# Optimization experiments

Hardware: AMD Instinct MI355X
Metric: run time of the kernel (lower is better)

The kernel has to match this reference:

```python
import jax, jax.numpy as jnp
import numpy as np

OBS_DIM, ACT_DIM, HID_DIM, FEAT = 256, 32, 1024, 512
T_STEPS, BATCH = 64, 512
LOG2PI = float(np.log(2.0 * np.pi))


def _mlp(h, w0, b0, w1, b1, w2, b2):
    # 2 hidden elu layers + linear head (MLPDecoder mean; fix_std Normal, std=1)
    x = jax.nn.elu(h @ w0.T + b0)
    x = jax.nn.elu(x @ w1.T + b1)
    return x @ w2.T + b2


def _gru(x, h, w_ih, w_hh, b_ih, b_hh):
    # torch.nn.GRUCell semantics
    gi = x @ w_ih.T + b_ih
    gh = h @ w_hh.T + b_hh
    i_r, i_z, i_n = jnp.split(gi, 3, axis=-1)
    h_r, h_z, h_n = jnp.split(gh, 3, axis=-1)
    r = jax.nn.sigmoid(i_r + h_r)
    z = jax.nn.sigmoid(i_z + h_z)
    n = jnp.tanh(i_n + r * h_n)
    return (1.0 - z) * n + z * h


def setup_inputs() -> dict:
    key = jax.random.key(0)
    ks = jax.random.split(key, 20)
    d = {}
    d['obs'] = jax.random.normal(ks[0], (T_STEPS, BATCH, OBS_DIM), jnp.float32)
    d['action'] = jax.random.normal(ks[1], (T_STEPS, BATCH, ACT_DIM), jnp.float32)
    d['reward'] = jax.random.normal(ks[2], (T_STEPS, BATCH, 1), jnp.float32)
    in_dim = OBS_DIM + ACT_DIM
    s = lambda fan_in: 1.0 / np.sqrt(fan_in)
    d['gru_w_ih'] = jax.random.normal(ks[3], (3 * HID_DIM, in_dim), jnp.float32) * s(in_dim)
    d['gru_w_hh'] = jax.random.normal(ks[4], (3 * HID_DIM, HID_DIM), jnp.float32) * s(HID_DIM)
    d['gru_b_ih'] = jnp.zeros((3 * HID_DIM,), jnp.float32)
    d['gru_b_hh'] = jnp.zeros((3 * HID_DIM,), jnp.float32)
    for name, out_dim, base in (('obs', OBS_DIM, 5), ('rew', 1, 11)):
        d[f'{name}_w0'] = jax.random.normal(ks[base], (FEAT, HID_DIM), jnp.float32) * s(HID_DIM)
        d[f'{name}_b0'] = jnp.zeros((FEAT,), jnp.float32)
        d[f'{name}_w1'] = jax.random.normal(ks[base + 1], (FEAT, FEAT), jnp.float32) * s(FEAT)
        d[f'{name}_b1'] = jnp.zeros((FEAT,), jnp.float32)
        d[f'{name}_w2'] = jax.random.normal(ks[base + 2], (out_dim, FEAT), jnp.float32) * s(FEAT)
        d[f'{name}_b2'] = jnp.zeros((out_dim,), jnp.float32)
    return d


def reference(obs, action, reward,
              gru_w_ih, gru_w_hh, gru_b_ih, gru_b_hh,
              obs_w0, obs_b0, obs_w1, obs_b1, obs_w2, obs_b2,
              rew_w0, rew_b0, rew_w1, rew_b1, rew_w2, rew_b2):
    T, B = obs.shape[0], obs.shape[1]

    def normal_logprob_sum(x, mean):
        # Normal(mean, std=1): -0.5*(x-mean)^2 - 0.5*log(2*pi), summed
        return -0.5 * jnp.sum((x - mean) ** 2 + LOG2PI)

    h0 = _gru(jnp.concatenate([obs[0], jnp.zeros_like(action[0])], axis=1),
              jnp.zeros((B, HID_DIM), obs.dtype),
              gru_w_ih, gru_w_hh, gru_b_ih, gru_b_hh)

    def step(h, xs):
        obs_t, act_t, rew_t = xs
        obs_mean = _mlp(h, obs_w0, obs_b0, obs_w1, obs_b1, obs_w2, obs_b2)
        lp_obs = normal_logprob_sum(obs_t, obs_mean)
        rew_mean = _mlp(h, rew_w0, rew_b0, rew_w1, rew_b1, rew_w2, rew_b2)
        lp_rew = normal_logprob_sum(rew_t, rew_mean)
        # feed predicted obs (mode) + ground-truth action back into the GRU
        x = jnp.concatenate([obs_mean, act_t], axis=1)
        h_next = _gru(x, h, gru_w_ih, gru_w_hh, gru_b_ih, gru_b_hh)
        return h_next, (obs_mean, rew_mean, lp_obs, lp_rew)

    _, (pre_obs, pre_reward, lp_obs, lp_rew) = jax.lax.scan(
        step, h0, (obs, action, reward))

    denom = jnp.asarray(T * B, obs.dtype)
    pre_obs_loss = -jnp.sum(lp_obs) / denom
    pre_reward_loss = -jnp.sum(lp_rew) / denom
    loss = pre_obs_loss + pre_reward_loss  # action_mimic=False -> action loss is 0
    return loss, pre_obs, pre_reward
```

## Files before the change

### kernel.cpp

```cpp
#include <hip/hip_runtime.h>
#include <stdint.h>

#define T_STEPS 64
#define BATCH   512
#define OBS_DIM 256
#define ACT_DIM 32
#define HID     1024
#define FEAT    512
#define GDIM    3072
#define KIH     288
#define NBLK    256
#define GMEMB   32
#define LOG2PI  1.8378770664093453f
#define HWREG_XCC_ID 14356

typedef __attribute__((ext_vector_type(8))) short  short8;
typedef __attribute__((ext_vector_type(4))) float  floatx4;
typedef __attribute__((ext_vector_type(4))) unsigned int uintx4;
typedef unsigned long long ull;

__device__ __forceinline__ float bf2f(unsigned int u) {
    return __uint_as_float(u << 16);
}
__device__ __forceinline__ unsigned int f2bf(float f) {
    unsigned int u = __float_as_uint(f);
    return (u + 0x7FFFu + ((u >> 16) & 1u)) >> 16;
}
__device__ __forceinline__ float elu1(float x)  { return x > 0.f ? x : expm1f(x); }
__device__ __forceinline__ float sigm(float x)  { return 1.f / (1.f + expf(-x)); }

__device__ __forceinline__ unsigned int dev_ld(const unsigned int* p) {
    return __hip_atomic_load(p, __ATOMIC_RELAXED, __HIP_MEMORY_SCOPE_AGENT);
}
__device__ __forceinline__ ull dev_ld64(const ull* p) {
    return __hip_atomic_load(p, __ATOMIC_RELAXED, __HIP_MEMORY_SCOPE_AGENT);
}
__device__ __forceinline__ void dev_st(unsigned int* p, unsigned int v) {
    __hip_atomic_store(p, v, __ATOMIC_RELAXED, __HIP_MEMORY_SCOPE_AGENT);
}
__device__ __forceinline__ float dev_ldf(const float* p) {
    return __uint_as_float(dev_ld((const unsigned int*)p));
}

template<bool COH>
__device__ __forceinline__ unsigned int a_ld(const unsigned int* p) {
    return COH ? dev_ld(p) : *p;
}
template<bool COH>
__device__ __forceinline__ ull a_ld64(const ull* p) {
    return COH ? dev_ld64(p) : *p;
}
template<bool COH>
__device__ __forceinline__ void a_st(unsigned int* p, unsigned int v) {
    if (COH) dev_st(p, v); else *p = v;
}

struct ParamsReal {
    const float* obs; const float* action; const float* reward;
    const float* b_ih; const float* b_hh;
    const float* b1o; const float* b1r; const float* b2o; const float* b2r;
    const unsigned short* Ws1; const unsigned short* Wih;
    const unsigned short* W1o; const unsigned short* W1r;
    const unsigned short* W2o; const unsigned short* w2r;
    const float* bias_s1;
    unsigned short* Z1[2]; unsigned short* Z2[2]; unsigned short* Xbuf[2];
    unsigned short* hbf[2]; unsigned short* GHb[2]; float* h[2];
    float* accum; float* out;
    int* bar;
};
#define P ParamsReal

__device__ __forceinline__ void bar_fast() {
    asm volatile("" ::: "memory");
    __builtin_amdgcn_s_barrier();
    asm volatile("" ::: "memory");
}
__device__ __forceinline__ void bar_lds() {
    asm volatile("s_waitcnt lgkmcnt(0)" ::: "memory");
    __builtin_amdgcn_s_barrier();
    asm volatile("" ::: "memory");
}

__device__ __forceinline__ void gbar(int* cnt, int* gen, int& epoch, int members) {
    __syncthreads();
    if (threadIdx.x == 0) {
        __builtin_amdgcn_fence(__ATOMIC_RELEASE, "workgroup");
        epoch++;
        int prev = __hip_atomic_fetch_add(cnt, 1, __ATOMIC_RELAXED,
                                          __HIP_MEMORY_SCOPE_AGENT);
        if (prev == members * epoch - 1) {
            __hip_atomic_store(gen, epoch, __ATOMIC_RELAXED,
                               __HIP_MEMORY_SCOPE_AGENT);
        } else {
            while (__hip_atomic_load(gen, __ATOMIC_RELAXED,
                                     __HIP_MEMORY_SCOPE_AGENT) < epoch)
                __builtin_amdgcn_s_sleep(2);
        }
        __builtin_amdgcn_fence(__ATOMIC_ACQUIRE, "workgroup");
    }
    __syncthreads();
}

template<bool COH>
__device__ __forceinline__ void s1_stage(const P& p, unsigned short* lds,
                                         int g, int m,
                                         const unsigned short* hbf_r,
                                         unsigned short* Z1_w,
                                         unsigned short* GHb_w) {
    const int tid = threadIdx.x, lane = tid & 63, wv = tid >> 6;
    const int wr = wv & 1, wc = wv >> 1, fr = lane & 15, fq = lane >> 4;
    const int rowg = g * 64, col0 = m * 128;
    unsigned short* ldsA = lds;
    unsigned short* ldsB = lds + 64 * 136;

    floatx4 acc[2][4];
    floatx4 z4 = {0.f, 0.f, 0.f, 0.f};
#pragma unroll
    for (int mi = 0; mi < 2; ++mi)
#pragma unroll
        for (int n = 0; n < 4; ++n) acc[mi][n] = z4;

    const ull* Aq = (const ull*)(hbf_r + (size_t)rowg * HID);
    const unsigned short* Bg = p.Ws1 + (size_t)col0 * HID;

    ull apf[8];
#pragma unroll
    for (int j = 0; j < 8; ++j) { int f = tid + 256 * j;
        apf[j] = a_ld64<COH>(Aq + (size_t)(f >> 5) * 256 + (f & 31)); }
    uintx4 rb0[4], rb1[4];
#pragma unroll
    for (int i = 0; i < 4; ++i) { int c = tid + 256 * i;
        const unsigned short* bp = Bg + (size_t)(c >> 3) * HID + ((c & 7) << 3);
        rb0[i] = __builtin_nontemporal_load((const uintx4*)bp);
        rb1[i] = __builtin_nontemporal_load((const uintx4*)(bp + 64)); }

#define S1_MFMA(ASUB)                                                          \
    {                                                                          \
        _Pragma("unroll")                                                      \
        for (int ks = 0; ks < 2; ++ks) {                                       \
            short8 af[2], bf8[4];                                              \
            _Pragma("unroll")                                                  \
            for (int mi = 0; mi < 2; ++mi)                                     \
                af[mi] = *(const short8*)(ldsA + (wr * 32 + mi * 16 + fr) * 136 + (ASUB) + ks * 32 + fq * 8); \
            _Pragma("unroll")                                                  \
            for (int n = 0; n < 4; ++n)                                        \
                bf8[n] = *(const short8*)(ldsB + (wc * 64 + n * 16 + fr) * 72 + ks * 32 + fq * 8); \
            _Pragma("unroll")                                                  \
            for (int mi = 0; mi < 2; ++mi)                                     \
                _Pragma("unroll")                                              \
                for (int n = 0; n < 4; ++n)                                    \
                    acc[mi][n] = __builtin_amdgcn_mfma_f32_16x16x32_bf16(      \
                        af[mi], bf8[n], acc[mi][n], 0, 0, 0);                  \
        }                                                                      \
// ... 36 lines not shown
    }
#undef S1_MFMA

    const bool isZ1 = (col0 < 1024);
#pragma unroll
    for (int mi = 0; mi < 2; ++mi)
#pragma unroll
        for (int n = 0; n < 4; ++n)
#pragma unroll
            for (int j = 0; j < 4; ++j) {
                int row = rowg + wr * 32 + mi * 16 + fq * 4 + j;
                int col = col0 + wc * 64 + n * 16 + fr;
                float v = acc[mi][n][j] + p.bias_s1[col];
                unsigned int ow = f2bf(isZ1 ? elu1(v) : v);
                unsigned int pr = __shfl_xor(ow, 1, 64);
                if (!(fr & 1)) {
                    unsigned int pk = ow | (pr << 16);
                    if (isZ1)
                        a_st<COH>((unsigned int*)(Z1_w + row * HID + col), pk);
                    else
                        a_st<COH>((unsigned int*)GHb_w + (size_t)row * 1536 + ((col - 1024) >> 1), pk);
                }
            }
}

template<bool COH>
__device__ __forceinline__ void s2_stage(const P& p, unsigned short* lds,
                                         int g, int m,
                                         const unsigned short* Z1_r,
                                         unsigned short* Z2_w) {
    const int tid = threadIdx.x, lane = tid & 63, wv = tid >> 6;
    const int wr = wv & 1, wc = wv >> 1, fr = lane & 15, fq = lane >> 4;
    const int rowg = g * 64;
    const int z = m >> 4, col0 = (m & 15) * 32;
    unsigned short* ldsA = lds;
    unsigned short* ldsB = lds + 64 * 136;

    floatx4 acc[2];
    floatx4 z4 = {0.f, 0.f, 0.f, 0.f};
    acc[0] = z4; acc[1] = z4;

    const ull* Aq = (const ull*)(Z1_r + (size_t)rowg * HID + z * FEAT);
    const unsigned short* Bg = (z ? p.W1r : p.W1o) + (size_t)col0 * FEAT;
    const float* bias = z ? p.b1r : p.b1o;

    ull apf[8];
#pragma unroll
    for (int j = 0; j < 8; ++j) { int f = tid + 256 * j;
        apf[j] = a_ld64<COH>(Aq + (size_t)(f >> 5) * 256 + (f & 31)); }
    const unsigned short* bp0 = Bg + (size_t)(tid >> 3) * FEAT + ((tid & 7) << 3);
    uintx4 rb0 = *(const uintx4*)(bp0);
    uintx4 rb1 = *(const uintx4*)(bp0 + 64);

#define S2_MFMA(ASUB)                                                          \
    {                                                                          \
        _Pragma("unroll")                                                      \
        for (int ks = 0; ks < 2; ++ks) {                                       \
            short8 bf8 = *(const short8*)(ldsB + (wc * 16 + fr) * 72 + ks * 32 + fq * 8); \
            _Pragma("unroll")                                                  \
            for (int mi = 0; mi < 2; ++mi) {                                   \
                short8 af = *(const short8*)(ldsA + (wr * 32 + mi * 16 + fr) * 136 + (ASUB) + ks * 32 + fq * 8); \
                acc[mi] = __builtin_amdgcn_mfma_f32_16x16x32_bf16(af, bf8, acc[mi], 0, 0, 0); \
            }                                                                  \
        }                                                                      \
    }

    for (int it2 = 0; it2 < 4; ++it2) {
        bar_fast();
#pragma unroll
        for (int j = 0; j < 8; ++j) { int f = tid + 256 * j;
            *(ull*)(ldsA + (size_t)(f >> 5) * 136 + ((f & 31) << 2)) = apf[j]; }
        *(uintx4*)(ldsB + (tid >> 3) * 72 + ((tid & 7) << 3)) = rb0;
        bar_lds();
        if (it2 < 3) {
            int c2 = it2 + 1;
#pragma unroll
            for (int j = 0; j < 8; ++j) { int f = tid + 256 * j;
                apf[j] = a_ld64<COH>(Aq + (size_t)(f >> 5) * 256 + c2 * 32 + (f & 31)); }
            rb0 = *(const uintx4*)(bp0 + (2 * it2 + 2) * 64);
        }
        S2_MFMA(0);
        bar_fast();
        *(uintx4*)(ldsB + (tid >> 3) * 72 + ((tid & 7) << 3)) = rb1;
        bar_lds();
        if (it2 < 3) rb1 = *(const uintx4*)(bp0 + (2 * it2 + 3) * 64);
        S2_MFMA(64);
    }
#undef S2_MFMA

#pragma unroll
    for (int mi = 0; mi < 2; ++mi)
#pragma unroll
        for (int j = 0; j < 4; ++j) {
            int row = rowg + wr * 32 + mi * 16 + fq * 4 + j;
            int col = col0 + wc * 16 + fr;
            float v = acc[mi][j] + bias[col];
            unsigned int ow = f2bf(elu1(v));
            unsigned int pr = __shfl_xor(ow, 1, 64);
            if (!(fr & 1))
                a_st<COH>((unsigned int*)(Z2_w + row * HID + z * FEAT + col), ow | (pr << 16));
        }
}

template<bool COH>
__device__ __forceinline__ void s3_stage(const P& p, unsigned short* lds,
                                         int g, int m, int t,
                                         const unsigned short* Z2_r,
                                         unsigned short* Xbuf_w) {
    const int tid = threadIdx.x, lane = tid & 63, wv = tid >> 6;
    const int wr = wv & 1, wc = wv >> 1, fr = lane & 15, fq = lane >> 4;
    const int rowg = g * 64;

    if (m < 8) {
        const int col0 = m * 32;
        unsigned short* ldsA = lds;
        unsigned short* ldsB = lds + 64 * 136;
        floatx4 acc[2];
        floatx4 z4 = {0.f, 0.f, 0.f, 0.f};
        acc[0] = z4; acc[1] = z4;

        const ull* Aq = (const ull*)(Z2_r + (size_t)rowg * HID);
        const unsigned short* Bg = p.W2o + (size_t)col0 * FEAT;

        ull apf[8];
#pragma unroll
        for (int j = 0; j < 8; ++j) { int f = tid + 256 * j;
            apf[j] = a_ld64<COH>(Aq + (size_t)(f >> 5) * 256 + (f & 31)); }
        const unsigned short* bp0 = Bg + (size_t)(tid >> 3) * FEAT + ((tid & 7) << 3);
        uintx4 rb0 = *(const uintx4*)(bp0);
        uintx4 rb1 = *(const uintx4*)(bp0 + 64);

#define S3_MFMA(ASUB)                                                          \
        {                                                                      \
            _Pragma("unroll")                                                  \
            for (int ks = 0; ks < 2; ++ks) {                                   \
                short8 bf8 = *(const short8*)(ldsB + (wc * 16 + fr) * 72 + ks * 32 + fq * 8); \
                _Pragma("unroll")                                              \
                for (int mi = 0; mi < 2; ++mi) {                               \
                    short8 af = *(const short8*)(ldsA + (wr * 32 + mi * 16 + fr) * 136 + (ASUB) + ks * 32 + fq * 8); \
                    acc[mi] = __builtin_amdgcn_mfma_f32_16x16x32_bf16(af, bf8, acc[mi], 0, 0, 0); \
                }                                                              \
            }                                                                  \
        }

        for (int it2 = 0; it2 < 4; ++it2) {
            bar_fast();
#pragma unroll
            for (int j = 0; j < 8; ++j) { int f = tid + 256 * j;
                *(ull*)(ldsA + (size_t)(f >> 5) * 136 + ((f & 31) << 2)) = apf[j]; }
            *(uintx4*)(ldsB + (tid >> 3) * 72 + ((tid & 7) << 3)) = rb0;
            bar_lds();
            if (it2 < 3) {
                int c2 = it2 + 1;
#pragma unroll
                for (int j = 0; j < 8; ++j) { int f = tid + 256 * j;
                    apf[j] = a_ld64<COH>(Aq + (size_t)(f >> 5) * 256 + c2 * 32 + (f & 31)); }
                rb0 = *(const uintx4*)(bp0 + (2 * it2 + 2) * 64);
            }
            S3_MFMA(0);
            bar_fast();
            *(uintx4*)(ldsB + (tid >> 3) * 72 + ((tid & 7) << 3)) = rb1;
            bar_lds();
            if (it2 < 3) rb1 = *(const uintx4*)(bp0 + (2 * it2 + 3) * 64);
            S3_MFMA(64);
        }
#undef S3_MFMA

        const int col = col0 + wc * 16 + fr;
        const float b2oc = p.b2o[col];
        float lsum = 0.f;
#pragma unroll
        for (int mi = 0; mi < 2; ++mi)
#pragma unroll
            for (int j = 0; j < 4; ++j) {
                int row = rowg + wr * 32 + mi * 16 + fq * 4 + j;
                float mval = acc[mi][j] + b2oc;
                size_t oidx = (size_t)t * BATCH * OBS_DIM + (size_t)row * OBS_DIM + col;
                __builtin_nontemporal_store(mval, p.out + 1 + oidx);
                unsigned int ow = f2bf(mval);
                unsigned int pr = __shfl_xor(ow, 1, 64);
                if (!(fr & 1))
                    a_st<COH>((unsigned int*)(Xbuf_w + row * KIH + col), ow | (pr << 16));
                float d = __builtin_nontemporal_load(p.obs + oidx) - mval;
                lsum += d * d;
            }
#pragma unroll
        for (int off = 32; off > 0; off >>= 1) lsum += __shfl_down(lsum, off, 64);
        if (lane == 0) atomicAdd(p.accum + 0, lsum);
    } else if (m == 8) {
        for (int e = tid; e < 64 * 16; e += 256) {
            int row = rowg + (e >> 4), cp = (e & 15) * 2;
            const float* ap = p.action + ((size_t)t * BATCH + row) * ACT_DIM + cp;
            unsigned int lo = f2bf(__builtin_nontemporal_load(ap));
            unsigned int hi = f2bf(__builtin_nontemporal_load(ap + 1));
            a_st<COH>((unsigned int*)(Xbuf_w + row * KIH + OBS_DIM + cp), lo | (hi << 16));
        }
    } else if (m >= 16) {
        const int row = rowg + (m - 16) * 4 + wv;
        const ull* zq = (const ull*)(Z2_r + (size_t)row * HID + FEAT) + lane * 2;
        ull z0 = a_ld64<COH>(zq);
        ull z1 = a_ld64<COH>(zq + 1);
        short8 w8 = *(const short8*)(p.w2r + lane * 8);
        float s = 0.f;
#pragma unroll
        for (int k = 0; k < 4; ++k) {
            unsigned int u = (unsigned int)(z0 >> (16 * k)) & 0xFFFFu;
            s += bf2f(u) * bf2f((unsigned int)(unsigned short)w8[k]);
        }
#pragma unroll
        for (int k = 0; k < 4; ++k) {
            unsigned int u = (unsigned int)(z1 >> (16 * k)) & 0xFFFFu;
            s += bf2f(u) * bf2f((unsigned int)(unsigned short)w8[4 + k]);
        }
#pragma unroll
        for (int off = 32; off > 0; off >>= 1) s += __shfl_down(s, off, 64);
        if (lane == 0) {
            float mm = s + p.b2r[0];
            __builtin_nontemporal_store(
                mm, p.out + 1 + (size_t)T_STEPS * BATCH * OBS_DIM + (size_t)t * BATCH + row);
            float d = __builtin_nontemporal_load(p.reward + (size_t)t * BATCH + row) - mm;
            atomicAdd(p.accum + 1, d * d);
        }
    }
}

template<bool COH>
__device__ __forceinline__ void s4_stage(const P& p, unsigned short* lds,
                                         int g, int m, int use_gh,
                                         const unsigned short* Xbuf_r,
                                         const unsigned short* GHb_r,
                                         const float* h_r,
                                         float* h_w, unsigned short* hbf_w) {
    const int tid = threadIdx.x, lane = tid & 63, wv = tid >> 6;
    const int wr = wv & 1, wc = wv >> 1, fr = lane & 15, fq = lane >> 4;
    const int rowg = g * 64;
    const int col0 = m * 32;
    unsigned short* ldsA = lds;
    unsigned short* ldsB = lds + 64 * 104;

    floatx4 acc[3][2];
    floatx4 z4 = {0.f, 0.f, 0.f, 0.f};
#pragma unroll
    for (int g3 = 0; g3 < 3; ++g3) { acc[g3][0] = z4; acc[g3][1] = z4; }

    const ull* Xq = (const ull*)(Xbuf_r + (size_t)rowg * KIH);
    ull apf[6];
#pragma unroll
    for (int j = 0; j < 6; ++j) { int f = tid + 256 * j;
        apf[j] = a_ld64<COH>(Xq + (size_t)(f / 24) * 72 + (f % 24)); }

    uintx4 wpfA[5], wpfB[5];
#pragma unroll
    for (int j = 0; j < 5; ++j) { int f = tid + 256 * j;
        if (f < 1152) { int r = f / 12, ko = (f - r * 12) * 8;
            const unsigned short* wp =
                p.Wih + (size_t)((r >> 5) * HID + col0 + (r & 31)) * KIH + ko;
            wpfA[j] = __builtin_nontemporal_load((const uintx4*)wp);
            wpfB[j] = __builtin_nontemporal_load((const uintx4*)(wp + 96)); } }

#pragma unroll
    for (int c = 0; c < 3; ++c) {
        bar_fast();
#pragma unroll
        for (int j = 0; j < 6; ++j) { int f = tid + 256 * j;
            *(ull*)(ldsA + (size_t)(f / 24) * 104 + ((f % 24) << 2)) = apf[j]; }
#pragma unroll
        for (int j = 0; j < 5; ++j) { int f = tid + 256 * j;
            if (f < 1152) { int r = f / 12, ko = (f - r * 12) * 8;
                *(uintx4*)(ldsB + r * 104 + ko) = (c & 1) ? wpfB[j] : wpfA[j]; } }
        bar_lds();
        if (c < 2) {
#pragma unroll
            for (int j = 0; j < 6; ++j) { int f = tid + 256 * j;
                apf[j] = a_ld64<COH>(Xq + (size_t)(f / 24) * 72 + (c + 1) * 24 + (f % 24)); }
        }
        if (c == 0) {
#pragma unroll
            for (int j = 0; j < 5; ++j) { int f = tid + 256 * j;
                if (f < 1152) { int r = f / 12, ko = (f - r * 12) * 8;
                    wpfA[j] = __builtin_nontemporal_load((const uintx4*)
                        (p.Wih + (size_t)((r >> 5) * HID + col0 + (r & 31)) * KIH + 192 + ko)); } }
        }
#pragma unroll
        for (int ks = 0; ks < 3; ++ks) {
            short8 af[2];
#pragma unroll
            for (int mi = 0; mi < 2; ++mi)
                af[mi] = *(const short8*)(ldsA + (wr * 32 + mi * 16 + fr) * 104 + ks * 32 + fq * 8);
#pragma unroll
            for (int g3 = 0; g3 < 3; ++g3) {
                short8 bf8 = *(const short8*)(ldsB + (g3 * 32 + wc * 16 + fr) * 104 + ks * 32 + fq * 8);
#pragma unroll
                for (int mi = 0; mi < 2; ++mi)
                    acc[g3][mi] = __builtin_amdgcn_mfma_f32_16x16x32_bf16(
                        af[mi], bf8, acc[g3][mi], 0, 0, 0);
            }
        }
    }

    const int col = col0 + wc * 16 + fr;
    const float bir = p.b_ih[col];
    const float biz = p.b_ih[HID + col];
    const float bin = p.b_ih[2 * HID + col];
    float hrv[2][4], hzv[2][4], hnv[2][4], hpv[2][4];
    if (use_gh) {
        const unsigned int* GW = (const unsigned int*)GHb_r;
        const int cw = col >> 1, hi = col & 1;
#pragma unroll
        for (int mi = 0; mi < 2; ++mi)
#pragma unroll
            for (int j = 0; j < 4; ++j) {
                int row = rowg + wr * 32 + mi * 16 + fq * 4 + j;
                unsigned int ur = a_ld<COH>(GW + (size_t)row * 1536 + cw);
                unsigned int uz = a_ld<COH>(GW + (size_t)row * 1536 + 512 + cw);
                unsigned int un = a_ld<COH>(GW + (size_t)row * 1536 + 1024 + cw);
                hrv[mi][j] = bf2f(hi ? (ur >> 16) : (ur & 0xFFFFu));
                hzv[mi][j] = bf2f(hi ? (uz >> 16) : (uz & 0xFFFFu));
                hnv[mi][j] = bf2f(hi ? (un >> 16) : (un & 0xFFFFu));
                hpv[mi][j] = __uint_as_float(a_ld<COH>((const unsigned int*)(h_r + (size_t)row * HID + col)));
            }
    } else {
        float br = p.b_hh[col], bz = p.b_hh[HID + col], bn = p.b_hh[2 * HID + col];
#pragma unroll
        for (int mi = 0; mi < 2; ++mi)
#pragma unroll
            for (int j = 0; j < 4; ++j) {
                hrv[mi][j] = br; hzv[mi][j] = bz; hnv[mi][j] = bn; hpv[mi][j] = 0.f;
            }
    }
#pragma unroll
    for (int mi = 0; mi < 2; ++mi)
#pragma unroll
        for (int j = 0; j < 4; ++j) {
            int row = rowg + wr * 32 + mi * 16 + fq * 4 + j;
            float r  = sigm(acc[0][mi][j] + bir + hrv[mi][j]);
            float z  = sigm(acc[1][mi][j] + biz + hzv[mi][j]);
            float nn = tanhf(acc[2][mi][j] + bin + r * hnv[mi][j]);
            float hv = (1.f - z) * nn + z * hpv[mi][j];
            a_st<COH>((unsigned int*)(h_w + (size_t)row * HID + col), __float_as_uint(hv));
            unsigned int ow = f2bf(hv);
            unsigned int pr = __shfl_xor(ow, 1, 64);
            if (!(fr & 1))
                a_st<COH>((unsigned int*)(hbf_w + row * HID + col), ow | (pr << 16));
        }
}

template<bool COH>
__device__ void rollout(const P& p, unsigned short* lds, int g, int m) {
    int* gcnt = p.bar + g * 128;
    int* ggen = p.bar + g * 128 + 64;
    int epoch = 0;

    s4_stage<COH>(p, lds, g, m, 0, p.Xbuf[1], p.GHb[0], p.h[0], p.h[0], p.hbf[0]);
    gbar(gcnt, ggen, epoch, GMEMB);

    for (int t = 0; t < T_STEPS; ++t) {
        const int pr = t & 1, nx = (t + 1) & 1;
        s1_stage<COH>(p, lds, g, m, p.hbf[pr], p.Z1[pr], p.GHb[pr]);
        gbar(gcnt, ggen, epoch, GMEMB);
        s2_stage<COH>(p, lds, g, m, p.Z1[pr], p.Z2[pr]);
        gbar(gcnt, ggen, epoch, GMEMB);
        s3_stage<COH>(p, lds, g, m, t, p.Z2[pr], p.Xbuf[pr]);
        gbar(gcnt, ggen, epoch, GMEMB);
        if (t < T_STEPS - 1) {
            s4_stage<COH>(p, lds, g, m, 1, p.Xbuf[pr], p.GHb[pr], p.h[pr],
                          p.h[nx], p.hbf[nx]);
            gbar(gcnt, ggen, epoch, GMEMB);
        }
    }
}

__global__ __launch_bounds__(256, 1) void k_persist(P p) {
    __shared__ unsigned short lds[17920];
    __shared__ int sh[3];

    const int bid = blockIdx.x;
    if (threadIdx.x == 0) {
        unsigned int xcd = __builtin_amdgcn_s_getreg(HWREG_XCC_ID) & 7u;
        int r = __hip_atomic_fetch_add(p.bar + 1024 + xcd, 1,
                                       __ATOMIC_RELAXED, __HIP_MEMORY_SCOPE_AGENT);
        sh[0] = (int)xcd; sh[1] = r;
    }
    int repoch = 0;
    gbar(p.bar + 1200, p.bar + 1264, repoch, NBLK);
    if (threadIdx.x == 0) {
        int ok = (sh[1] < 32);
        for (int i = 0; i < 8; ++i)
            ok &= (dev_ld((const unsigned int*)(p.bar + 1024 + i)) == 32u);
        sh[2] = ok;
    }
    __syncthreads();

    if (sh[2]) rollout<false>(p, lds, sh[0], sh[1]);
    else       rollout<true >(p, lds, bid & 7, bid >> 3);

    gbar(p.bar + 1200, p.bar + 1264, repoch, NBLK);
    if (bid == 0 && threadIdx.x == 0) {
        const float inv = 1.f / (float)(T_STEPS * BATCH);
        float a0 = dev_ldf(p.accum + 0);
        float a1 = dev_ldf(p.accum + 1);
        p.out[0] = 0.5f * a0 * inv + 128.f * LOG2PI
                 + 0.5f * a1 * inv + 0.5f * LOG2PI;
    }
}

__global__ void k_convert(
    const float* __restrict__ ow0, const float* __restrict__ rw0,
    const float* __restrict__ whh, const float* __restrict__ wih,
    const float* __restrict__ ow1, const float* __restrict__ rw1,
    const float* __restrict__ ow2, const float* __restrict__ rw2,
    const float* __restrict__ ob0, const float* __restrict__ rb0,
    const float* __restrict__ bhh,
    unsigned short* __restrict__ Ws1, unsigned short* __restrict__ Wih,
    unsigned short* __restrict__ W1o, unsigned short* __restrict__ W1r,
    unsigned short* __restrict__ W2o, unsigned short* __restrict__ w2r,
    float* __restrict__ bias_s1)
{
    const int i0 = blockIdx.x * 256 + threadIdx.x;
    const int stride = gridDim.x * 256;
    for (int i = i0; i < 4096 * 1024; i += stride) {
        int row = i >> 10;
        float v = (row < 512) ? ow0[i]
                : (row < 1024) ? rw0[i - 512 * 1024]
                               : whh[i - 1024 * 1024];
        Ws1[i] = (unsigned short)f2bf(v);
    }
    for (int i = i0; i < GDIM * KIH; i += stride) Wih[i] = (unsigned short)f2bf(wih[i]);
    for (int i = i0; i < FEAT * FEAT; i += stride) {
        W1o[i] = (unsigned short)f2bf(ow1[i]);
        W1r[i] = (unsigned short)f2bf(rw1[i]);
    }
    for (int i = i0; i < OBS_DIM * FEAT; i += stride) W2o[i] = (unsigned short)f2bf(ow2[i]);
    for (int i = i0; i < FEAT; i += stride) w2r[i] = (unsigned short)f2bf(rw2[i]);
    for (int i = i0; i < 4096; i += stride)
        bias_s1[i] = (i < 512) ? ob0[i] : (i < 1024) ? rb0[i - 512] : bhh[i - 1024];
}

__global__ void k_init(const float* __restrict__ obs,
                       unsigned short* __restrict__ Xbuf1,
                       float* __restrict__ accum,
                       int* __restrict__ bar)
{
    int i = blockIdx.x * 256 + threadIdx.x;
    if (i < BATCH * KIH) {
        int row = i / KIH, col = i - row * KIH;
        Xbuf1[i] = (col < OBS_DIM) ? (unsigned short)f2bf(obs[row * OBS_DIM + col])
                                   : (unsigned short)0;
    }
    if (i < 2)    accum[i] = 0.f;
    if (i < 1536) bar[i] = 0;
}

extern "C" void kernel_launch(void* const* d_in, const int* in_sizes, int n_in,
                              void* d_out, int out_size, void* d_ws, size_t ws_size,
                              hipStream_t stream)
{
    const float* obs      = (const float*)d_in[0];
    const float* action   = (const float*)d_in[1];
    const float* reward   = (const float*)d_in[2];
    const float* gru_w_ih = (const float*)d_in[3];
    const float* gru_w_hh = (const float*)d_in[4];
    const float* gru_b_ih = (const float*)d_in[5];
    const float* gru_b_hh = (const float*)d_in[6];
    const float* obs_w0   = (const float*)d_in[7];
    const float* obs_b0   = (const float*)d_in[8];
    const float* obs_w1   = (const float*)d_in[9];
    const float* obs_b1   = (const float*)d_in[10];
    const float* obs_w2   = (const float*)d_in[11];
    const float* obs_b2   = (const float*)d_in[12];
    const float* rew_w0   = (const float*)d_in[13];
    const float* rew_b0   = (const float*)d_in[14];
    const float* rew_w1   = (const float*)d_in[15];
    const float* rew_b1   = (const float*)d_in[16];
    const float* rew_w2   = (const float*)d_in[17];
    const float* rew_b2   = (const float*)d_in[18];

    char* ws = (char*)d_ws;
    auto alloc = [&](size_t bytes) -> char* {
        char* pr = ws;
        ws += (bytes + 255) & ~(size_t)255;
        return pr;
    };
    unsigned short* Ws1  = (unsigned short*)alloc((size_t)4096 * 1024 * 2);
    unsigned short* Wih  = (unsigned short*)alloc((size_t)GDIM * KIH * 2);
    unsigned short* W1o  = (unsigned short*)alloc((size_t)FEAT * FEAT * 2);
    unsigned short* W1r  = (unsigned short*)alloc((size_t)FEAT * FEAT * 2);
    unsigned short* W2o  = (unsigned short*)alloc((size_t)OBS_DIM * FEAT * 2);
    unsigned short* w2r  = (unsigned short*)alloc((size_t)FEAT * 2);
    float* bias_s1       = (float*)alloc((size_t)4096 * 4);
    unsigned short* Z1a  = (unsigned short*)alloc((size_t)BATCH * HID * 2);
    unsigned short* Z1b  = (unsigned short*)alloc((size_t)BATCH * HID * 2);
    unsigned short* Z2a  = (unsigned short*)alloc((size_t)BATCH * HID * 2);
    unsigned short* Z2b  = (unsigned short*)alloc((size_t)BATCH * HID * 2);
    unsigned short* GHa  = (unsigned short*)alloc((size_t)BATCH * GDIM * 2);
    unsigned short* GHbB = (unsigned short*)alloc((size_t)BATCH * GDIM * 2);
    unsigned short* Xba  = (unsigned short*)alloc((size_t)BATCH * KIH * 2);
    unsigned short* Xbb  = (unsigned short*)alloc((size_t)BATCH * KIH * 2);
    float* ha            = (float*)alloc((size_t)BATCH * HID * 4);
    float* hb            = (float*)alloc((size_t)BATCH * HID * 4);
    unsigned short* hfa  = (unsigned short*)alloc((size_t)BATCH * HID * 2);
    unsigned short* hfb  = (unsigned short*)alloc((size_t)BATCH * HID * 2);
    float* accum         = (float*)alloc(256);
    int*   bar           = (int*)alloc(8192);

    dim3 blk(256);

    k_convert<<<dim3(1024), blk, 0, stream>>>(
        obs_w0, rew_w0, gru_w_hh, gru_w_ih, obs_w1, rew_w1, obs_w2, rew_w2,
        obs_b0, rew_b0, gru_b_hh, Ws1, Wih, W1o, W1r, W2o, w2r, bias_s1);

    k_init<<<dim3((BATCH * KIH + 255) / 256), blk, 0, stream>>>(obs, Xbb, accum, bar);

    P hp;
    hp.obs = obs; hp.action = action; hp.reward = reward;
    hp.b_ih = gru_b_ih; hp.b_hh = gru_b_hh;
    hp.b1o = obs_b1; hp.b1r = rew_b1; hp.b2o = obs_b2; hp.b2r = rew_b2;
    hp.Ws1 = Ws1; hp.Wih = Wih; hp.W1o = W1o; hp.W1r = W1r;
    hp.W2o = W2o; hp.w2r = w2r; hp.bias_s1 = bias_s1;
    hp.Z1[0] = Z1a; hp.Z1[1] = Z1b;
    hp.Z2[0] = Z2a; hp.Z2[1] = Z2b;
    hp.Xbuf[0] = Xba; hp.Xbuf[1] = Xbb;
    hp.hbf[0] = hfa; hp.hbf[1] = hfb;
    hp.GHb[0] = GHa; hp.GHb[1] = GHbB;
    hp.h[0] = ha; hp.h[1] = hb;
    hp.accum = accum; hp.out = (float*)d_out;
    hp.bar = bar;

    k_persist<<<dim3(NBLK), blk, 0, stream>>>(hp);
}
```

Baseline: 2.542 ms.

## Fold obs head into GRU input weights and overlap head stage with GRU update

Precomputes a fused weight Wf = W_ih[:, :256]·W2o, plus a folded bias, in the convert kernel. The GRU input-gate GEMM can then read the second hidden layer Z2 directly instead of waiting for the obs-mean output stage. The s3 head/loss stage now runs between arrive and wait of a split flag barrier, so one full grid barrier per step leaves the critical path. The atomic counter barrier is replaced with per-block flag slots, and double buffers are collapsed to single buffers. In exchange the GRU input GEMM K grows from 288 to 544, setup runs a naive fp32 weight-product loop, and bf16 rounding of the folded weights changes numerics slightly.

```diff
diff --git a/kernel.cpp b/kernel.cpp
--- a/kernel.cpp
+++ b/kernel.cpp
@@ -9,6 +9,7 @@
 #define FEAT    512
 #define GDIM    3072
 #define KIH     288
+#define KF      544
 #define NBLK    256
 #define GMEMB   32
 #define LOG2PI  1.8378770664093453f
@@ -62,9 +63,10 @@
     const unsigned short* Ws1; const unsigned short* Wih;
     const unsigned short* W1o; const unsigned short* W1r;
     const unsigned short* W2o; const unsigned short* w2r;
+    const unsigned short* Wf;  const float* bf_fold;
     const float* bias_s1;
-    unsigned short* Z1[2]; unsigned short* Z2[2]; unsigned short* Xbuf[2];
-    unsigned short* hbf[2]; unsigned short* GHb[2]; float* h[2];
+    unsigned short* Z1; unsigned short* Z2; unsigned short* Xbuf1;
+    unsigned short* hbf; unsigned short* GHb; float* h[2];
     float* accum; float* out;
     int* bar;
 };
@@ -99,6 +101,28 @@
         __builtin_amdgcn_fence(__ATOMIC_ACQUIRE, "workgroup");
     }
     __syncthreads();
+}
+
+__device__ __forceinline__ void arrive_flags(int* fbase, int m, int epoch) {
+    __syncthreads();
+    if (threadIdx.x == 0) {
+        __builtin_amdgcn_fence(__ATOMIC_RELEASE, "workgroup");
+        dev_st((unsigned int*)(fbase + m * 16), (unsigned int)epoch);
+    }
+}
+__device__ __forceinline__ void wait_flags(int* fbase, int epoch) {
+    if (threadIdx.x < 64) {
+        const unsigned int* fp =
+            (const unsigned int*)(fbase + (threadIdx.x & 31) * 16);
+        while ((int)dev_ld(fp) < epoch) __builtin_amdgcn_s_sleep(4);
+        __builtin_amdgcn_fence(__ATOMIC_ACQUIRE, "workgroup");
+    }
+    __syncthreads();
+}
+__device__ __forceinline__ void gbar_flags(int* fbase, int m, int& epoch) {
+    epoch++;
+    arrive_flags(fbase, m, epoch);
+    wait_flags(fbase, epoch);
 }
 
 template<bool COH>
@@ -241,18 +265,16 @@
     uintx4 rb0 = *(const uintx4*)(bp0);
     uintx4 rb1 = *(const uintx4*)(bp0 + 64);
 
-#define S2_MFMA(ASUB)                                                          \
-    {                                                                          \
+#define S23_MFMA(ASUB)                                                         \
+    { _Pragma("unroll")                                                        \
+      for (int ks = 0; ks < 2; ++ks) {                                         \
+        short8 bf8 = *(const short8*)(ldsB + (wc * 16 + fr) * 72 + ks * 32 + fq * 8); \
         _Pragma("unroll")                                                      \
-        for (int ks = 0; ks < 2; ++ks) {                                       \
-            short8 bf8 = *(const short8*)(ldsB + (wc * 16 + fr) * 72 + ks * 32 + fq * 8); \
-            _Pragma("unroll")                                                  \
-            for (int mi = 0; mi < 2; ++mi) {                                   \
-                short8 af = *(const short8*)(ldsA + (wr * 32 + mi * 16 + fr) * 136 + (ASUB) + ks * 32 + fq * 8); \
-                acc[mi] = __builtin_amdgcn_mfma_f32_16x16x32_bf16(af, bf8, acc[mi], 0, 0, 0); \
-            }                                                                  \
+        for (int mi = 0; mi < 2; ++mi) {                                       \
+            short8 af = *(const short8*)(ldsA + (wr * 32 + mi * 16 + fr) * 136 + (ASUB) + ks * 32 + fq * 8); \
+            acc[mi] = __builtin_amdgcn_mfma_f32_16x16x32_bf16(af, bf8, acc[mi], 0, 0, 0); \
         }                                                                      \
-    }
+      } }
 
     for (int it2 = 0; it2 < 4; ++it2) {
         bar_fast();
@@ -268,14 +290,13 @@
                 apf[j] = a_ld64<COH>(Aq + (size_t)(f >> 5) * 256 + c2 * 32 + (f & 31)); }
             rb0 = *(const uintx4*)(bp0 + (2 * it2 + 2) * 64);
         }
-        S2_MFMA(0);
+        S23_MFMA(0);
         bar_fast();
         *(uintx4*)(ldsB + (tid >> 3) * 72 + ((tid & 7) << 3)) = rb1;
         bar_lds();
         if (it2 < 3) rb1 = *(const uintx4*)(bp0 + (2 * it2 + 3) * 64);
-        S2_MFMA(64);
-    }
-#undef S2_MFMA
+        S23_MFMA(64);
+    }
 
 #pragma unroll
     for (int mi = 0; mi < 2; ++mi)
@@ -294,10 +315,10 @@
 template<bool COH>
 __device__ __forceinline__ void s3_stage(const P& p, unsigned short* lds,
                                          int g, int m, int t,
-                                         const unsigned short* Z2_r,
-                                         unsigned short* Xbuf_w) {
+                                         const unsigned short* Z2_r) {
     const int tid = threadIdx.x, lane = tid & 63, wv = tid >> 6;
-    const int wr = wv & 1, wc = wv >> 1, fr = lane & 15, fq = lane >> 4;
+    const int wr = wv & 1, wc = wv >> 1;
+    const int fr = lane & 15, fq = lane >> 4;
     const int rowg = g * 64;
 
     if (m < 8) {
@@ -319,19 +340,6 @@
         uintx4 rb0 = *(const uintx4*)(bp0);
         uintx4 rb1 = *(const uintx4*)(bp0 + 64);
 
-#define S3_MFMA(ASUB)                                                          \
-        {                                                                      \
-            _Pragma("unroll")                                                  \
-            for (int ks = 0; ks < 2; ++ks) {                                   \
-                short8 bf8 = *(const short8*)(ldsB + (wc * 16 + fr) * 72 + ks * 32 + fq * 8); \
-                _Pragma("unroll")                                              \
-                for (int mi = 0; mi < 2; ++mi) {                               \
-                    short8 af = *(const short8*)(ldsA + (wr * 32 + mi * 16 + fr) * 136 + (ASUB) + ks * 32 + fq * 8); \
-                    acc[mi] = __builtin_amdgcn_mfma_f32_16x16x32_bf16(af, bf8, acc[mi], 0, 0, 0); \
-                }                                                              \
-            }                                                                  \
-        }
-
         for (int it2 = 0; it2 < 4; ++it2) {
             bar_fast();
 #pragma unroll
@@ -346,14 +354,13 @@
                     apf[j] = a_ld64<COH>(Aq + (size_t)(f >> 5) * 256 + c2 * 32 + (f & 31)); }
                 rb0 = *(const uintx4*)(bp0 + (2 * it2 + 2) * 64);
             }
-            S3_MFMA(0);
+            S23_MFMA(0);
             bar_fast();
             *(uintx4*)(ldsB + (tid >> 3) * 72 + ((tid & 7) << 3)) = rb1;
             bar_lds();
             if (it2 < 3) rb1 = *(const uintx4*)(bp0 + (2 * it2 + 3) * 64);
-            S3_MFMA(64);
-        }
-#undef S3_MFMA
+            S23_MFMA(64);
+        }
 
         const int col = col0 + wc * 16 + fr;
         const float b2oc = p.b2o[col];
@@ -366,24 +373,12 @@
                 float mval = acc[mi][j] + b2oc;
                 size_t oidx = (size_t)t * BATCH * OBS_DIM + (size_t)row * OBS_DIM + col;
                 __builtin_nontemporal_store(mval, p.out + 1 + oidx);
-                unsigned int ow = f2bf(mval);
-                unsigned int pr = __shfl_xor(ow, 1, 64);
-                if (!(fr & 1))
-                    a_st<COH>((unsigned int*)(Xbuf_w + row * KIH + col), ow | (pr << 16));
                 float d = __builtin_nontemporal_load(p.obs + oidx) - mval;
                 lsum += d * d;
             }
 #pragma unroll
         for (int off = 32; off > 0; off >>= 1) lsum += __shfl_down(lsum, off, 64);
         if (lane == 0) atomicAdd(p.accum + 0, lsum);
-    } else if (m == 8) {
-        for (int e = tid; e < 64 * 16; e += 256) {
-            int row = rowg + (e >> 4), cp = (e & 15) * 2;
-            const float* ap = p.action + ((size_t)t * BATCH + row) * ACT_DIM + cp;
-            unsigned int lo = f2bf(__builtin_nontemporal_load(ap));
-            unsigned int hi = f2bf(__builtin_nontemporal_load(ap + 1));
-            a_st<COH>((unsigned int*)(Xbuf_w + row * KIH + OBS_DIM + cp), lo | (hi << 16));
-        }
     } else if (m >= 16) {
         const int row = rowg + (m - 16) * 4 + wv;
         const ull* zq = (const ull*)(Z2_r + (size_t)row * HID + FEAT) + lane * 2;
@@ -414,85 +409,134 @@
 }
 
 template<bool COH>
-__device__ __forceinline__ void s4_stage(const P& p, unsigned short* lds,
-                                         int g, int m, int use_gh,
-                                         const unsigned short* Xbuf_r,
-                                         const unsigned short* GHb_r,
-                                         const float* h_r,
-                                         float* h_w, unsigned short* hbf_w) {
+__device__ __forceinline__ void s4f_stage(const P& p, unsigned short* lds,
+                                          int g, int m, int t,
+                                          const unsigned short* Z2_r,
+                                          const unsigned short* GHb_r,
+                                          const float* h_r,
+                                          float* h_w, unsigned short* hbf_w) {
     const int tid = threadIdx.x, lane = tid & 63, wv = tid >> 6;
-    const int wr = wv & 1, wc = wv >> 1, fr = lane & 15, fq = lane >> 4;
+    const int wr = wv & 1, wc = wv >> 1;
+    const int fr = lane & 15, fq = lane >> 4;
     const int rowg = g * 64;
     const int col0 = m * 32;
     unsigned short* ldsA = lds;
-    unsigned short* ldsB = lds + 64 * 104;
+    unsigned short* ldsB = lds + 64 * 136;
 
     floatx4 acc[3][2];
     floatx4 z4 = {0.f, 0.f, 0.f, 0.f};
 #pragma unroll
     for (int g3 = 0; g3 < 3; ++g3) { acc[g3][0] = z4; acc[g3][1] = z4; }
 
-    const ull* Xq = (const ull*)(Xbuf_r + (size_t)rowg * KIH);
-    ull apf[6];
-#pragma unroll
-    for (int j = 0; j < 6; ++j) { int f = tid + 256 * j;
-        apf[j] = a_ld64<COH>(Xq + (size_t)(f / 24) * 72 + (f % 24)); }
-
-    uintx4 wpfA[5], wpfB[5];
-#pragma unroll
-    for (int j = 0; j < 5; ++j) { int f = tid + 256 * j;
-        if (f < 1152) { int r = f / 12, ko = (f - r * 12) * 8;
-            const unsigned short* wp =
-                p.Wih + (size_t)((r >> 5) * HID + col0 + (r & 31)) * KIH + ko;
-            wpfA[j] = __builtin_nontemporal_load((const uintx4*)wp);
-            wpfB[j] = __builtin_nontemporal_load((const uintx4*)(wp + 96)); } }
-
-#pragma unroll
-    for (int c = 0; c < 3; ++c) {
+    const ull* Aq = (const ull*)(Z2_r + (size_t)rowg * HID);
+
+    ull apf[8];
+#pragma unroll
+    for (int j = 0; j < 8; ++j) { int f = tid + 256 * j;
+        apf[j] = a_ld64<COH>(Aq + (size_t)(f >> 5) * 256 + (f & 31)); }
+    uintx4 rb0[3], rb1[3];
+#pragma unroll
+    for (int i = 0; i < 3; ++i) { int c = tid + 256 * i;
+        int r = c >> 3, ko = (c & 7) << 3;
+        const unsigned short* bp =
+            p.Wf + (size_t)((r >> 5) * HID + col0 + (r & 31)) * KF + ko;
+        rb0[i] = __builtin_nontemporal_load((const uintx4*)bp);
+        rb1[i] = __builtin_nontemporal_load((const uintx4*)(bp + 64)); }
+
+#define S4F_MFMA(ASUB)                                                         \
+    { _Pragma("unroll")                                                        \
+      for (int ks = 0; ks < 2; ++ks) {                                         \
+        short8 af[2];                                                          \
+        _Pragma("unroll")                                                      \
+        for (int mi = 0; mi < 2; ++mi)                                         \
+            af[mi] = *(const short8*)(ldsA + (wr * 32 + mi * 16 + fr) * 136 + (ASUB) + ks * 32 + fq * 8); \
+        _Pragma("unroll")                                                      \
+        for (int g3 = 0; g3 < 3; ++g3) {                                       \
+            short8 bf8 = *(const short8*)(ldsB + (g3 * 32 + wc * 16 + fr) * 72 + ks * 32 + fq * 8); \
+            _Pragma("unroll")                                                  \
+            for (int mi = 0; mi < 2; ++mi)                                     \
+                acc[g3][mi] = __builtin_amdgcn_mfma_f32_16x16x32_bf16(         \
+                    af[mi], bf8, acc[g3][mi], 0, 0, 0);                        \
+        }                                                                      \
+      } }
+
+    for (int it2 = 0; it2 < 4; ++it2) {
         bar_fast();
 #pragma unroll
-        for (int j = 0; j < 6; ++j) { int f = tid + 256 * j;
-            *(ull*)(ldsA + (size_t)(f / 24) * 104 + ((f % 24) << 2)) = apf[j]; }
-#pragma unroll
-        for (int j = 0; j < 5; ++j) { int f = tid + 256 * j;
-            if (f < 1152) { int r = f / 12, ko = (f - r * 12) * 8;
-                *(uintx4*)(ldsB + r * 104 + ko) = (c & 1) ? wpfB[j] : wpfA[j]; } }
+        for (int j = 0; j < 8; ++j) { int f = tid + 256 * j;
+            *(ull*)(ldsA + (size_t)(f >> 5) * 136 + ((f & 31) << 2)) = apf[j]; }
+#pragma unroll
+        for (int i = 0; i < 3; ++i) { int c = tid + 256 * i;
+            int r = c >> 3, ko = (c & 7) << 3;
+            *(uintx4*)(ldsB + r * 72 + ko) = rb0[i]; }
         bar_lds();
-        if (c < 2) {
-#pragma unroll
-            for (int j = 0; j < 6; ++j) { int f = tid + 256 * j;
-                apf[j] = a_ld64<COH>(Xq + (size_t)(f / 24) * 72 + (c + 1) * 24 + (f % 24)); }
-        }
-        if (c == 0) {
-#pragma unroll
-            for (int j = 0; j < 5; ++j) { int f = tid + 256 * j;
-                if (f < 1152) { int r = f / 12, ko = (f - r * 12) * 8;
-                    wpfA[j] = __builtin_nontemporal_load((const uintx4*)
-                        (p.Wih + (size_t)((r >> 5) * HID + col0 + (r & 31)) * KIH + 192 + ko)); } }
-        }
-#pragma unroll
-        for (int ks = 0; ks < 3; ++ks) {
-            short8 af[2];
+        if (it2 < 3) {
+            int c2 = it2 + 1;
+#pragma unroll
+            for (int j = 0; j < 8; ++j) { int f = tid + 256 * j;
+                apf[j] = a_ld64<COH>(Aq + (size_t)(f >> 5) * 256 + c2 * 32 + (f & 31)); }
+#pragma unroll
+            for (int i = 0; i < 3; ++i) { int c = tid + 256 * i;
+                int r = c >> 3, ko = (c & 7) << 3;
+                rb0[i] = __builtin_nontemporal_load((const uintx4*)
+                    (p.Wf + (size_t)((r >> 5) * HID + col0 + (r & 31)) * KF
+                     + (2 * it2 + 2) * 64 + ko)); }
+        }
+        S4F_MFMA(0);
+        bar_fast();
+#pragma unroll
+        for (int i = 0; i < 3; ++i) { int c = tid + 256 * i;
+            int r = c >> 3, ko = (c & 7) << 3;
+            *(uintx4*)(ldsB + r * 72 + ko) = rb1[i]; }
+        bar_lds();
+        if (it2 < 3) {
+#pragma unroll
+            for (int i = 0; i < 3; ++i) { int c = tid + 256 * i;
+                int r = c >> 3, ko = (c & 7) << 3;
+                rb1[i] = __builtin_nontemporal_load((const uintx4*)
+                    (p.Wf + (size_t)((r >> 5) * HID + col0 + (r & 31)) * KF
+                     + (2 * it2 + 3) * 64 + ko)); }
+        }
+        S4F_MFMA(64);
+    }
+
+    bar_fast();
+    for (int e = tid; e < 64 * 32; e += 256) {
+        int row = e >> 5, cc = e & 31;
+        float av = __builtin_nontemporal_load(
+            p.action + ((size_t)t * BATCH + rowg + row) * ACT_DIM + cc);
+        ldsA[row * 136 + cc] = (unsigned short)f2bf(av);
+    }
+#pragma unroll
+    for (int i = 0; i < 2; ++i) { int c = tid + 256 * i;
+        if (c < 384) {
+            int r = c >> 2, ko = (c & 3) << 3;
+            *(uintx4*)(ldsB + r * 72 + ko) = __builtin_nontemporal_load((const uintx4*)
+                (p.Wf + (size_t)((r >> 5) * HID + col0 + (r & 31)) * KF + 512 + ko));
+        } }
+    bar_lds();
+    {
+        short8 af[2];
+#pragma unroll
+        for (int mi = 0; mi < 2; ++mi)
+            af[mi] = *(const short8*)(ldsA + (wr * 32 + mi * 16 + fr) * 136 + fq * 8);
+#pragma unroll
+        for (int g3 = 0; g3 < 3; ++g3) {
+            short8 bf8 = *(const short8*)(ldsB + (g3 * 32 + wc * 16 + fr) * 72 + fq * 8);
 #pragma unroll
             for (int mi = 0; mi < 2; ++mi)
-                af[mi] = *(const short8*)(ldsA + (wr * 32 + mi * 16 + fr) * 104 + ks * 32 + fq * 8);
-#pragma unroll
-            for (int g3 = 0; g3 < 3; ++g3) {
-                short8 bf8 = *(const short8*)(ldsB + (g3 * 32 + wc * 16 + fr) * 104 + ks * 32 + fq * 8);
-#pragma unroll
-                for (int mi = 0; mi < 2; ++mi)
-                    acc[g3][mi] = __builtin_amdgcn_mfma_f32_16x16x32_bf16(
-                        af[mi], bf8, acc[g3][mi], 0, 0, 0);
-            }
-        }
-    }
+                acc[g3][mi] = __builtin_amdgcn_mfma_f32_16x16x32_bf16(
+                    af[mi], bf8, acc[g3][mi], 0, 0, 0);
+        }
+    }
+#undef S4F_MFMA
 
     const int col = col0 + wc * 16 + fr;
-    const float bir = p.b_ih[col];
-    const float biz = p.b_ih[HID + col];
-    const float bin = p.b_ih[2 * HID + col];
+    const float bir = p.b_ih[col]           + p.bf_fold[col];
+    const float biz = p.b_ih[HID + col]     + p.bf_fold[HID + col];
+    const float bin = p.b_ih[2 * HID + col] + p.bf_fold[2 * HID + col];
     float hrv[2][4], hzv[2][4], hnv[2][4], hpv[2][4];
-    if (use_gh) {
+    {
         const unsigned int* GW = (const unsigned int*)GHb_r;
         const int cw = col >> 1, hi = col & 1;
 #pragma unroll
@@ -507,14 +551,6 @@
                 hzv[mi][j] = bf2f(hi ? (uz >> 16) : (uz & 0xFFFFu));
                 hnv[mi][j] = bf2f(hi ? (un >> 16) : (un & 0xFFFFu));
                 hpv[mi][j] = __uint_as_float(a_ld<COH>((const unsigned int*)(h_r + (size_t)row * HID + col)));
-            }
-    } else {
-        float br = p.b_hh[col], bz = p.b_hh[HID + col], bn = p.b_hh[2 * HID + col];
-#pragma unroll
-        for (int mi = 0; mi < 2; ++mi)
-#pragma unroll
-            for (int j = 0; j < 4; ++j) {
-                hrv[mi][j] = br; hzv[mi][j] = bz; hnv[mi][j] = bn; hpv[mi][j] = 0.f;
             }
     }
 #pragma unroll
@@ -535,26 +571,122 @@
 }
 
 template<bool COH>
+__device__ __forceinline__ void s4_stage(const P& p, unsigned short* lds,
+                                         int g, int m,
+                                         const unsigned short* Xbuf_r,
+                                         float* h_w, unsigned short* hbf_w) {
+    const int tid = threadIdx.x, lane = tid & 63, wv = tid >> 6;
+    const int wr = wv & 1, wc = wv >> 1;
+    const int fr = lane & 15, fq = lane >> 4;
+    const int rowg = g * 64;
+    const int col0 = m * 32;
+    unsigned short* ldsA = lds;
+    unsigned short* ldsB = lds + 64 * 104;
+
+    floatx4 acc[3][2];
+    floatx4 z4 = {0.f, 0.f, 0.f, 0.f};
+#pragma unroll
+    for (int g3 = 0; g3 < 3; ++g3) { acc[g3][0] = z4; acc[g3][1] = z4; }
+
+    const ull* Xq = (const ull*)(Xbuf_r + (size_t)rowg * KIH);
+    ull apf[6];
+#pragma unroll
+    for (int j = 0; j < 6; ++j) { int f = tid + 256 * j;
+        apf[j] = a_ld64<COH>(Xq + (size_t)(f / 24) * 72 + (f % 24)); }
+
+    uintx4 wpfA[5], wpfB[5];
+#pragma unroll
+    for (int j = 0; j < 5; ++j) { int f = tid + 256 * j;
+        if (f < 1152) { int r = f / 12, ko = (f - r * 12) * 8;
+            const unsigned short* wp =
+                p.Wih + (size_t)((r >> 5) * HID + col0 + (r & 31)) * KIH + ko;
+            wpfA[j] = __builtin_nontemporal_load((const uintx4*)wp);
+            wpfB[j] = __builtin_nontemporal_load((const uintx4*)(wp + 96)); } }
+
+#pragma unroll
+    for (int c = 0; c < 3; ++c) {
+        bar_fast();
+#pragma unroll
+        for (int j = 0; j < 6; ++j) { int f = tid + 256 * j;
+            *(ull*)(ldsA + (size_t)(f / 24) * 104 + ((f % 24) << 2)) = apf[j]; }
+#pragma unroll
+        for (int j = 0; j < 5; ++j) { int f = tid + 256 * j;
+            if (f < 1152) { int r = f / 12, ko = (f - r * 12) * 8;
+                *(uintx4*)(ldsB + r * 104 + ko) = (c & 1) ? wpfB[j] : wpfA[j]; } }
+        bar_lds();
+        if (c < 2) {
+#pragma unroll
+            for (int j = 0; j < 6; ++j) { int f = tid + 256 * j;
+                apf[j] = a_ld64<COH>(Xq + (size_t)(f / 24) * 72 + (c + 1) * 24 + (f % 24)); }
+        }
+        if (c == 0) {
+#pragma unroll
+            for (int j = 0; j < 5; ++j) { int f = tid + 256 * j;
+                if (f < 1152) { int r = f / 12, ko = (f - r * 12) * 8;
+                    wpfA[j] = __builtin_nontemporal_load((const uintx4*)
+                        (p.Wih + (size_t)((r >> 5) * HID + col0 + (r & 31)) * KIH + 192 + ko)); } }
+        }
+#pragma unroll
+        for (int ks = 0; ks < 3; ++ks) {
+            short8 af[2];
+#pragma unroll
+            for (int mi = 0; mi < 2; ++mi)
+                af[mi] = *(const short8*)(ldsA + (wr * 32 + mi * 16 + fr) * 104 + ks * 32 + fq * 8);
+#pragma unroll
+            for (int g3 = 0; g3 < 3; ++g3) {
+                short8 bf8 = *(const short8*)(ldsB + (g3 * 32 + wc * 16 + fr) * 104 + ks * 32 + fq * 8);
+#pragma unroll
+                for (int mi = 0; mi < 2; ++mi)
+                    acc[g3][mi] = __builtin_amdgcn_mfma_f32_16x16x32_bf16(
+                        af[mi], bf8, acc[g3][mi], 0, 0, 0);
+            }
+        }
+    }
+
+    const int col = col0 + wc * 16 + fr;
+    const float bir = p.b_ih[col];
+    const float biz = p.b_ih[HID + col];
+    const float bin = p.b_ih[2 * HID + col];
+    const float br = p.b_hh[col], bz = p.b_hh[HID + col], bn = p.b_hh[2 * HID + col];
+#pragma unroll
+    for (int mi = 0; mi < 2; ++mi)
+#pragma unroll
+        for (int j = 0; j < 4; ++j) {
+            int row = rowg + wr * 32 + mi * 16 + fq * 4 + j;
+            float r  = sigm(acc[0][mi][j] + bir + br);
+            float z  = sigm(acc[1][mi][j] + biz + bz);
+            float nn = tanhf(acc[2][mi][j] + bin + r * bn);
+            float hv = (1.f - z) * nn;
+            a_st<COH>((unsigned int*)(h_w + (size_t)row * HID + col), __float_as_uint(hv));
+            unsigned int ow = f2bf(hv);
+            unsigned int pr = __shfl_xor(ow, 1, 64);
+            if (!(fr & 1))
+                a_st<COH>((unsigned int*)(hbf_w + row * HID + col), ow | (pr << 16));
+        }
+}
+
+template<bool COH>
 __device__ void rollout(const P& p, unsigned short* lds, int g, int m) {
-    int* gcnt = p.bar + g * 128;
-    int* ggen = p.bar + g * 128 + 64;
-    int epoch = 0;
-
-    s4_stage<COH>(p, lds, g, m, 0, p.Xbuf[1], p.GHb[0], p.h[0], p.h[0], p.hbf[0]);
-    gbar(gcnt, ggen, epoch, GMEMB);
+    int* fbase = p.bar + 2048 + g * 512;
+    int fep = 0;
+
+    s4_stage<COH>(p, lds, g, m, p.Xbuf1, p.h[0], p.hbf);
+    gbar_flags(fbase, m, fep);
 
     for (int t = 0; t < T_STEPS; ++t) {
-        const int pr = t & 1, nx = (t + 1) & 1;
-        s1_stage<COH>(p, lds, g, m, p.hbf[pr], p.Z1[pr], p.GHb[pr]);
-        gbar(gcnt, ggen, epoch, GMEMB);
-        s2_stage<COH>(p, lds, g, m, p.Z1[pr], p.Z2[pr]);
-        gbar(gcnt, ggen, epoch, GMEMB);
-        s3_stage<COH>(p, lds, g, m, t, p.Z2[pr], p.Xbuf[pr]);
-        gbar(gcnt, ggen, epoch, GMEMB);
+        s1_stage<COH>(p, lds, g, m, p.hbf, p.Z1, p.GHb);
+        gbar_flags(fbase, m, fep);
+        s2_stage<COH>(p, lds, g, m, p.Z1, p.Z2);
+        gbar_flags(fbase, m, fep);
         if (t < T_STEPS - 1) {
-            s4_stage<COH>(p, lds, g, m, 1, p.Xbuf[pr], p.GHb[pr], p.h[pr],
-                          p.h[nx], p.hbf[nx]);
-            gbar(gcnt, ggen, epoch, GMEMB);
+            s4f_stage<COH>(p, lds, g, m, t, p.Z2, p.GHb, p.h[t & 1],
+                           p.h[(t + 1) & 1], p.hbf);
+            fep++;
+            arrive_flags(fbase, m, fep);
+            s3_stage<COH>(p, lds, g, m, t, p.Z2);
+            wait_flags(fbase, fep);
+        } else {
+            s3_stage<COH>(p, lds, g, m, t, p.Z2);
         }
     }
 }
@@ -599,10 +731,11 @@
     const float* __restrict__ ow1, const float* __restrict__ rw1,
     const float* __restrict__ ow2, const float* __restrict__ rw2,
     const float* __restrict__ ob0, const float* __restrict__ rb0,
-    const float* __restrict__ bhh,
+    const float* __restrict__ bhh, const float* __restrict__ ob2,
     unsigned short* __restrict__ Ws1, unsigned short* __restrict__ Wih,
     unsigned short* __restrict__ W1o, unsigned short* __restrict__ W1r,
     unsigned short* __restrict__ W2o, unsigned short* __restrict__ w2r,
+    unsigned short* __restrict__ Wf,  float* __restrict__ bf_fold,
     float* __restrict__ bias_s1)
 {
     const int i0 = blockIdx.x * 256 + threadIdx.x;
@@ -623,6 +756,25 @@
     for (int i = i0; i < FEAT; i += stride) w2r[i] = (unsigned short)f2bf(rw2[i]);
     for (int i = i0; i < 4096; i += stride)
         bias_s1[i] = (i < 512) ? ob0[i] : (i < 1024) ? rb0[i - 512] : bhh[i - 1024];
+    for (int i = i0; i < GDIM * 512; i += stride) {
+        int r = i >> 9, f = i & 511;
+        const float* wr_ = wih + (size_t)r * KIH;
+        const float* w2c = ow2 + f;
+        float s = 0.f;
+        for (int o = 0; o < 256; ++o) s += wr_[o] * w2c[(size_t)o * 512];
+        Wf[(size_t)r * KF + f] = (unsigned short)f2bf(s);
+    }
+    for (int i = i0; i < GDIM * 32; i += stride) {
+        int r = i >> 5, c = i & 31;
+        Wf[(size_t)r * KF + 512 + c] =
+            (unsigned short)f2bf(wih[(size_t)r * KIH + 256 + c]);
+    }
+    for (int i = i0; i < GDIM; i += stride) {
+        const float* wr_ = wih + (size_t)i * KIH;
+        float s = 0.f;
+        for (int o = 0; o < 256; ++o) s += wr_[o] * ob2[o];
+        bf_fold[i] = s;
+    }
 }
 
 __global__ void k_init(const float* __restrict__ obs,
@@ -637,7 +789,7 @@
                                    : (unsigned short)0;
     }
     if (i < 2)    accum[i] = 0.f;
-    if (i < 1536) bar[i] = 0;
+    if (i < 8192) bar[i] = 0;
 }
 
 extern "C" void kernel_launch(void* const* d_in, const int* in_sizes, int n_in,
@@ -676,44 +828,38 @@
     unsigned short* W1r  = (unsigned short*)alloc((size_t)FEAT * FEAT * 2);
     unsigned short* W2o  = (unsigned short*)alloc((size_t)OBS_DIM * FEAT * 2);
     unsigned short* w2r  = (unsigned short*)alloc((size_t)FEAT * 2);
+    unsigned short* Wf   = (unsigned short*)alloc((size_t)GDIM * KF * 2);
+    float* bf_fold       = (float*)alloc((size_t)GDIM * 4);
     float* bias_s1       = (float*)alloc((size_t)4096 * 4);
-    unsigned short* Z1a  = (unsigned short*)alloc((size_t)BATCH * HID * 2);
-    unsigned short* Z1b  = (unsigned short*)alloc((size_t)BATCH * HID * 2);
-    unsigned short* Z2a  = (unsigned short*)alloc((size_t)BATCH * HID * 2);
-    unsigned short* Z2b  = (unsigned short*)alloc((size_t)BATCH * HID * 2);
-    unsigned short* GHa  = (unsigned short*)alloc((size_t)BATCH * GDIM * 2);
-    unsigned short* GHbB = (unsigned short*)alloc((size_t)BATCH * GDIM * 2);
-    unsigned short* Xba  = (unsigned short*)alloc((size_t)BATCH * KIH * 2);
-    unsigned short* Xbb  = (unsigned short*)alloc((size_t)BATCH * KIH * 2);
+    unsigned short* Z1   = (unsigned short*)alloc((size_t)BATCH * HID * 2);
+    unsigned short* Z2   = (unsigned short*)alloc((size_t)BATCH * HID * 2);
+    unsigned short* GHb  = (unsigned short*)alloc((size_t)BATCH * GDIM * 2);
+    unsigned short* Xb1  = (unsigned short*)alloc((size_t)BATCH * KIH * 2);
     float* ha            = (float*)alloc((size_t)BATCH * HID * 4);
     float* hb            = (float*)alloc((size_t)BATCH * HID * 4);
-    unsigned short* hfa  = (unsigned short*)alloc((size_t)BATCH * HID * 2);
-    unsigned short* hfb  = (unsigned short*)alloc((size_t)BATCH * HID * 2);
+    unsigned short* hf   = (unsigned short*)alloc((size_t)BATCH * HID * 2);
     float* accum         = (float*)alloc(256);
-    int*   bar           = (int*)alloc(8192);
-
-    dim3 blk(256);
-
-    k_convert<<<dim3(1024), blk, 0, stream>>>(
+    int*   bar           = (int*)alloc(32768);
+
+    k_convert<<<dim3(1024), dim3(256), 0, stream>>>(
         obs_w0, rew_w0, gru_w_hh, gru_w_ih, obs_w1, rew_w1, obs_w2, rew_w2,
-        obs_b0, rew_b0, gru_b_hh, Ws1, Wih, W1o, W1r, W2o, w2r, bias_s1);
-
-    k_init<<<dim3((BATCH * KIH + 255) / 256), blk, 0, stream>>>(obs, Xbb, accum, bar);
+        obs_b0, rew_b0, gru_b_hh, obs_b2,
+        Ws1, Wih, W1o, W1r, W2o, w2r, Wf, bf_fold, bias_s1);
+
+    k_init<<<dim3((BATCH * KIH + 255) / 256), dim3(256), 0, stream>>>(obs, Xb1, accum, bar);
 
     P hp;
     hp.obs = obs; hp.action = action; hp.reward = reward;
     hp.b_ih = gru_b_ih; hp.b_hh = gru_b_hh;
     hp.b1o = obs_b1; hp.b1r = rew_b1; hp.b2o = obs_b2; hp.b2r = rew_b2;
     hp.Ws1 = Ws1; hp.Wih = Wih; hp.W1o = W1o; hp.W1r = W1r;
-    hp.W2o = W2o; hp.w2r = w2r; hp.bias_s1 = bias_s1;
-    hp.Z1[0] = Z1a; hp.Z1[1] = Z1b;
-    hp.Z2[0] = Z2a; hp.Z2[1] = Z2b;
-    hp.Xbuf[0] = Xba; hp.Xbuf[1] = Xbb;
-    hp.hbf[0] = hfa; hp.hbf[1] = hfb;
-    hp.GHb[0] = GHa; hp.GHb[1] = GHbB;
+    hp.W2o = W2o; hp.w2r = w2r; hp.Wf = Wf; hp.bf_fold = bf_fold;
+    hp.bias_s1 = bias_s1;
+    hp.Z1 = Z1; hp.Z2 = Z2; hp.Xbuf1 = Xb1;
+    hp.hbf = hf; hp.GHb = GHb;
     hp.h[0] = ha; hp.h[1] = hb;
     hp.accum = accum; hp.out = (float*)d_out;
     hp.bar = bar;
 
-    k_persist<<<dim3(NBLK), blk, 0, stream>>>(hp);
-}
+    k_persist<<<dim3(NBLK), dim3(256), 0, stream>>>(hp);
+}
```

Result: slower. 4.466 ms (+75.7%).
